# Optimization experiments

Measured on AMD Instinct MI355X. Metric: run time of the kernel, lower is better.

## Reference

```python
import jax, jax.numpy as jnp
import numpy as np

B, POMO, PROB, EMB, H, D = 64, 200, 200, 512, 16, 32
SQRT_EMB = 22.627416997969522  # sqrt(512)
CLIP = 10.0


def _heads(x):
    # (b, n, H*D) -> (b, H, n, D)
    b, n, _ = x.shape
    return x.reshape(b, n, H, D).transpose(0, 2, 1, 3)


def setup_inputs() -> dict:
    key = jax.random.key(0)
    ks = jax.random.split(key, 10)
    s = 1.0 / np.sqrt(EMB)
    return {
        "encoded_nodes": jax.random.normal(ks[0], (B, PROB + 1, EMB), jnp.float32),
        "encoded_q1": jax.random.normal(ks[1], (B, POMO, EMB), jnp.float32),
        "encoded_last_node": jax.random.normal(ks[2], (B, POMO, EMB), jnp.float32),
        "ninf_mask": jnp.zeros((B, POMO, PROB), jnp.float32),
        "Wq_first": jax.random.normal(ks[3], (EMB, H * D), jnp.float32) * s,
        "Wq_last": jax.random.normal(ks[4], (EMB, H * D), jnp.float32) * s,
        "Wk": jax.random.normal(ks[5], (EMB, H * D), jnp.float32) * s,
        "Wv": jax.random.normal(ks[6], (EMB, H * D), jnp.float32) * s,
        "Wc": jax.random.normal(ks[7], (H * D, EMB), jnp.float32) * s,
        "bc": jax.random.normal(ks[8], (EMB,), jnp.float32) * 0.01,
    }


def reference(encoded_nodes, encoded_q1, encoded_last_node, ninf_mask,
              Wq_first, Wq_last, Wk, Wv, Wc, bc):
    # set_kv
    k = _heads(encoded_nodes @ Wk)            # (b, H, prob+1, D)
    v = _heads(encoded_nodes @ Wv)            # (b, H, prob+1, D)
    single_head_key = encoded_nodes[:, :-1]   # (b, prob, emb)
    # set_q1 + forward queries
    q = _heads(encoded_q1 @ Wq_first) + _heads(encoded_last_node @ Wq_last)  # (b, H, pomo, D)
    # masked multi-head attention; mask padded with a zero column for the depot/last node
    mask3 = jnp.concatenate([ninf_mask, jnp.zeros((B, POMO, 1), ninf_mask.dtype)], axis=-1)
    score = jnp.einsum('bhnd,bhmd->bhnm', q, k) / jnp.sqrt(jnp.float32(D))
    weights = jax.nn.softmax(score + mask3[:, None, :, :], axis=-1)
    out = jnp.einsum('bhnm,bhmd->bhnd', weights, v)        # (b, H, pomo, D)
    out_concat = out.transpose(0, 2, 1, 3).reshape(B, POMO, H * D)
    mh_atten_out = out_concat @ Wc + bc                    # (b, pomo, emb)
    # single-head pointer score with tanh clipping
    score2 = jnp.einsum('bne,bpe->bnp', mh_atten_out, single_head_key) / SQRT_EMB
    score_masked = CLIP * jnp.tanh(score2) + ninf_mask
    return jax.nn.softmax(score_masked, axis=2)            # (b, pomo, prob)
```

## Files before the change

kernel.cpp:

```cpp
#include <hip/hip_runtime.h>
#include <cstdint>
#include <cstddef>

typedef _Float16 f16;
typedef f16 f16x4 __attribute__((ext_vector_type(4)));
typedef f16 f16x8 __attribute__((ext_vector_type(8)));
typedef float f32x4 __attribute__((ext_vector_type(4)));

#define NB    64
#define NPOMO 200
#define NNODE 201
#define NEMB  512
#define NH    16
#define ND    32

__device__ __forceinline__ void gload16(const void* g, void* l) {
  __builtin_amdgcn_global_load_lds((const __attribute__((address_space(1))) void*)g,
                                   (__attribute__((address_space(3))) void*)l, 16, 0, 0);
}


__global__ void cast_x(const float* __restrict__ x, f16* __restrict__ o, int n4) {
  int i = blockIdx.x * 256 + threadIdx.x;
  if (i < n4) {
    float4 v = ((const float4*)x)[i];
    f16x4 h = {(f16)v.x, (f16)v.y, (f16)v.z, (f16)v.w};
    ((f16x4*)o)[i] = h;
  }
}

__global__ void build_qcat(const float* __restrict__ q1, const float* __restrict__ ql,
                           f16* __restrict__ o) {
  int i = blockIdx.x * 256 + threadIdx.x;
  if (i >= 12800 * 256) return;
  int row = i >> 8;
  int g = i & 255;
  const float* src = (g < 128) ? (q1 + (size_t)row * 512 + g * 4)
                               : (ql + (size_t)row * 512 + (g - 128) * 4);
  float4 v = *(const float4*)src;
  f16x4 h = {(f16)v.x, (f16)v.y, (f16)v.z, (f16)v.w};
  ((f16x4*)o)[i] = h;
}

__global__ void build_w(const float* __restrict__ Wk, const float* __restrict__ Wv,
                        const float* __restrict__ Wqf, const float* __restrict__ Wql,
                        const float* __restrict__ Wc,
                        f16* __restrict__ wkvT, f16* __restrict__ wqT, f16* __restrict__ wcT) {
  int i = blockIdx.x * 256 + threadIdx.x;
  if (i < 524288) {
    int j = i >> 9, k = i & 511;
    float v = (j < 512) ? Wk[(size_t)k * 512 + j] : Wv[(size_t)k * 512 + (j - 512)];
    wkvT[i] = (f16)v;
  } else if (i < 1048576) {
    int t = i - 524288;
    int j = t >> 10, k = t & 1023;
    float v = (k < 512) ? Wqf[(size_t)k * 512 + j] : Wql[(size_t)(k - 512) * 512 + j];
    wqT[t] = (f16)v;
  } else if (i < 1310720) {
    int t = i - 1048576;
    int j = t >> 9, k = t & 511;
    wcT[t] = (f16)Wc[(size_t)k * 512 + j];
  }
}


__global__ __launch_bounds__(256, 2) void gemm_tn(
    const f16* __restrict__ A, const f16* __restrict__ B, f16* __restrict__ C,
    const float* __restrict__ bias, int M, int N, int K) {
  __shared__ f16 As[128 * 64];
  __shared__ f16 Bs[128 * 64];
  const int tid = threadIdx.x;
  const int wave = tid >> 6, lane = tid & 63;
  const int qd = lane >> 4, c = lane & 15;
  const int wm = wave >> 1, wn = wave & 1;
  const int m0 = blockIdx.x * 128, n0 = blockIdx.y * 128;
  const int srow = lane >> 3, sj = lane & 7;

  f32x4 acc[4][4];
#pragma unroll
  for (int i = 0; i < 4; ++i)
#pragma unroll
    for (int j = 0; j < 4; ++j) acc[i][j] = (f32x4){0.f, 0.f, 0.f, 0.f};

  for (int kc = 0; kc < K; kc += 64) {
#pragma unroll
    for (int i = 0; i < 4; ++i) {
      int row = wave * 32 + i * 8 + srow;
      int gr = m0 + row; if (gr >= M) gr = M - 1;
      int gj = sj ^ (row & 7);
      gload16(A + (size_t)gr * K + kc + gj * 8, As + row * 64 + sj * 8);
    }
#pragma unroll
    for (int i = 0; i < 4; ++i) {
      int row = wave * 32 + i * 8 + srow;
      int gj = sj ^ (row & 7);
      gload16(B + (size_t)(n0 + row) * K + kc + gj * 8, Bs + row * 64 + sj * 8);
    }
    __syncthreads();
#pragma unroll
    for (int kk = 0; kk < 2; ++kk) {
      f16x8 af[4], bf[4];
#pragma unroll
      for (int t = 0; t < 4; ++t) {
        int ra = wm * 64 + t * 16 + c;
        af[t] = *(const f16x8*)(As + ra * 64 + (((kk * 4 + qd) ^ (ra & 7)) * 8));
        int rb = wn * 64 + t * 16 + c;
        bf[t] = *(const f16x8*)(Bs + rb * 64 + (((kk * 4 + qd) ^ (rb & 7)) * 8));
      }
#pragma unroll
      for (int mt = 0; mt < 4; ++mt)
#pragma unroll
        for (int nt = 0; nt < 4; ++nt)
          acc[mt][nt] = __builtin_amdgcn_mfma_f32_16x16x32_f16(af[mt], bf[nt], acc[mt][nt], 0, 0, 0);
    }
    __syncthreads();
  }

#pragma unroll
  for (int mt = 0; mt < 4; ++mt) {
#pragma unroll
    for (int nt = 0; nt < 4; ++nt) {
      int col = n0 + wn * 64 + nt * 16 + c;
      float bv = bias ? bias[col] : 0.0f;
#pragma unroll
      for (int r = 0; r < 4; ++r) {
        int row = m0 + wm * 64 + mt * 16 + qd * 4 + r;
        if (row < M) C[(size_t)row * N + col] = (f16)(acc[mt][nt][r] + bv);
      }
    }
  }
}


#define VSTR 268

__global__ __launch_bounds__(256, 4) void attn_kernel(
    const f16* __restrict__ Qp, const f16* __restrict__ KV,
    const float* __restrict__ mask, f16* __restrict__ Oc) {
  __shared__ f16 Vt[32 * VSTR];
  const int bid = blockIdx.x;
  const int qq = bid & 3;
  const int h = (bid >> 2) & 15;
  const int b = bid >> 6;
  const int tid = threadIdx.x;
  const int wave = tid >> 6, lane = tid & 63;
  const int qd = lane >> 4, c = lane & 15;

  for (int idx = tid; idx < 208 * 8; idx += 256) {
    int m = idx >> 3, ch = idx & 7;
    f16x4 v = (f16x4){0, 0, 0, 0};
    if (m < 201) v = *(const f16x4*)(KV + ((size_t)(b * NNODE + m)) * 1024 + 512 + h * 32 + ch * 4);
    Vt[(ch * 4 + 0) * VSTR + m] = v.x;
    Vt[(ch * 4 + 1) * VSTR + m] = v.y;
    Vt[(ch * 4 + 2) * VSTR + m] = v.z;
    Vt[(ch * 4 + 3) * VSTR + m] = v.w;
  }
  __syncthreads();

  const int start = (qq == 0) ? 0 : (1 + 3 * qq);
  const int ntile = (qq == 0) ? 4 : 3;
  const int rt = start + wave;
  if (wave >= ntile) return;

  const int r0 = rt * 16;
  const int qrow = min(r0 + c, 199);
  const float scale = 0.17677669529663687f;

  f16x8 aq = *(const f16x8*)(Qp + ((size_t)(b * NPOMO + qrow)) * 512 + h * 32 + qd * 8);

  f32x4 s[13];
#pragma unroll
  for (int nt = 0; nt < 13; ++nt) {
    int node = nt * 16 + c; if (node > 200) node = 200;
    f16x8 ak = *(const f16x8*)(KV + ((size_t)(b * NNODE + node)) * 1024 + h * 32 + qd * 8);
    f32x4 z = (f32x4){0.f, 0.f, 0.f, 0.f};
    s[nt] = __builtin_amdgcn_mfma_f32_16x16x32_f16(ak, aq, z, 0, 0, 0);
  }

  float mx = -3e38f;
#pragma unroll
  for (int nt = 0; nt < 13; ++nt) {
    const int col0 = nt * 16 + qd * 4;
    float4 mv = make_float4(0.f, 0.f, 0.f, 0.f);
    if (col0 < 200)
      mv = *(const float4*)(mask + ((size_t)b * NPOMO + qrow) * 200 + col0);
#pragma unroll
    for (int r = 0; r < 4; ++r) {
      int node = col0 + r;
      float v;
      if (node > 200)      v = -3e38f;
      else if (node == 200) v = s[nt][r] * scale;
      else                  v = s[nt][r] * scale + ((const float*)&mv)[r];
      s[nt][r] = v;
      mx = fmaxf(mx, v);
    }
  }
  mx = fmaxf(mx, __shfl_xor(mx, 16));
  mx = fmaxf(mx, __shfl_xor(mx, 32));

  float sm = 0.f;
  f16x4 pf[13];
#pragma unroll
  for (int nt = 0; nt < 13; ++nt) {
    f16x4 p4;
#pragma unroll
    for (int r = 0; r < 4; ++r) {
      float p = __expf(s[nt][r] - mx);
      sm += p;
      p4[r] = (f16)p;
    }
    pf[nt] = p4;
  }
  sm += __shfl_xor(sm, 16);
  sm += __shfl_xor(sm, 32);
  const float inv = 1.0f / sm;

  f32x4 o0 = (f32x4){0.f, 0.f, 0.f, 0.f};
  f32x4 o1 = (f32x4){0.f, 0.f, 0.f, 0.f};
#pragma unroll
  for (int nt = 0; nt < 13; ++nt) {
    const int nb = nt * 16 + qd * 4;
    f16x4 av0 = *(const f16x4*)(Vt + c * VSTR + nb);
    f16x4 av1 = *(const f16x4*)(Vt + (c + 16) * VSTR + nb);
    o0 = __builtin_amdgcn_mfma_f32_16x16x16f16(av0, pf[nt], o0, 0, 0, 0);
    o1 = __builtin_amdgcn_mfma_f32_16x16x16f16(av1, pf[nt], o1, 0, 0, 0);
  }

  const int row = r0 + c;
  if (row < 200) {
    f16* dst = Oc + ((size_t)(b * NPOMO + row)) * 512 + h * 32 + qd * 4;
    f16x4 w0 = {(f16)(o0[0] * inv), (f16)(o0[1] * inv), (f16)(o0[2] * inv), (f16)(o0[3] * inv)};
    f16x4 w1 = {(f16)(o1[0] * inv), (f16)(o1[1] * inv), (f16)(o1[2] * inv), (f16)(o1[3] * inv)};
    *(f16x4*)dst = w0;
    *(f16x4*)(dst + 16) = w1;
  }
}


__global__ __launch_bounds__(256, 2) void final_kernel(
    const f16* __restrict__ mh, const f16* __restrict__ Xnh,
    const float* __restrict__ mask, float* __restrict__ out) {
  __shared__ f16 As[64 * 72];
  __shared__ f16 Bs[208 * 72];
  const int b = blockIdx.x >> 2, rb = blockIdx.x & 3;
  const int r0 = rb * 64;
  const int tid = threadIdx.x;
  const int wave = tid >> 6, lane = tid & 63;
  const int qd = lane >> 4, c = lane & 15;

  f32x4 acc[13];
#pragma unroll
  for (int i = 0; i < 13; ++i) acc[i] = (f32x4){0.f, 0.f, 0.f, 0.f};

  for (int kc = 0; kc < 512; kc += 64) {
    for (int idx = tid; idx < 64 * 16; idx += 256) {
      int row = idx >> 4, ch = idx & 15;
      int gr = r0 + row; if (gr > 199) gr = 199;
      *(f16x4*)(As + row * 72 + ch * 4) =
          *(const f16x4*)(mh + ((size_t)b * NPOMO + gr) * 512 + kc + ch * 4);
    }
    for (int idx = tid; idx < 208 * 16; idx += 256) {
      int n = idx >> 4, ch = idx & 15;
      f16x4 v = (f16x4){0, 0, 0, 0};
      if (n < 200) v = *(const f16x4*)(Xnh + ((size_t)b * NNODE + n) * 512 + kc + ch * 4);
      *(f16x4*)(Bs + n * 72 + ch * 4) = v;
    }
    __syncthreads();
#pragma unroll
    for (int kk = 0; kk < 2; ++kk) {
      f16x8 a = *(const f16x8*)(As + (wave * 16 + c) * 72 + kk * 32 + qd * 8);
#pragma unroll
      for (int nt = 0; nt < 13; ++nt) {
        f16x8 bb = *(const f16x8*)(Bs + (nt * 16 + c) * 72 + kk * 32 + qd * 8);
        acc[nt] = __builtin_amdgcn_mfma_f32_16x16x32_f16(a, bb, acc[nt], 0, 0, 0);
      }
    }
    __syncthreads();
  }

  const float invS = 1.0f / 22.627416997969522f;
  const int rowb = r0 + wave * 16 + qd * 4;
  float mx[4] = {-3e38f, -3e38f, -3e38f, -3e38f};
#pragma unroll
  for (int nt = 0; nt < 13; ++nt) {
    int col = nt * 16 + c;
#pragma unroll
    for (int r = 0; r < 4; ++r) {
      float v;
      if (col < 200) {
        v = 10.0f * tanhf(acc[nt][r] * invS);
        int rr = rowb + r;
        if (rr < 200) v += mask[((size_t)b * NPOMO + rr) * 200 + col];
      } else {
        v = -3e38f;
      }
      acc[nt][r] = v;
      mx[r] = fmaxf(mx[r], v);
    }
  }
#pragma unroll
  for (int off = 8; off >= 1; off >>= 1)
#pragma unroll
    for (int r = 0; r < 4; ++r) mx[r] = fmaxf(mx[r], __shfl_xor(mx[r], off, 16));
  float sm[4] = {0.f, 0.f, 0.f, 0.f};
#pragma unroll
  for (int nt = 0; nt < 13; ++nt)
#pragma unroll
    for (int r = 0; r < 4; ++r) {
      float p = __expf(acc[nt][r] - mx[r]);
      acc[nt][r] = p;
      sm[r] += p;
    }
#pragma unroll
  for (int off = 8; off >= 1; off >>= 1)
#pragma unroll
    for (int r = 0; r < 4; ++r) sm[r] += __shfl_xor(sm[r], off, 16);
  float inv[4];
#pragma unroll
  for (int r = 0; r < 4; ++r) inv[r] = 1.0f / sm[r];
#pragma unroll
  for (int nt = 0; nt < 13; ++nt) {
    int col = nt * 16 + c;
#pragma unroll
    for (int r = 0; r < 4; ++r) {
      int rr = rowb + r;
      if (col < 200 && rr < 200)
        out[((size_t)b * NPOMO + rr) * 200 + col] = acc[nt][r] * inv[r];
    }
  }
}


extern "C" void kernel_launch(void* const* d_in, const int* in_sizes, int n_in,
                              void* d_out, int out_size, void* d_ws, size_t ws_size,
                              hipStream_t stream) {
  (void)in_sizes; (void)n_in; (void)out_size; (void)ws_size;
  const float* enc   = (const float*)d_in[0];
  const float* q1    = (const float*)d_in[1];
  const float* qlast = (const float*)d_in[2];
  const float* mask  = (const float*)d_in[3];
  const float* Wqf   = (const float*)d_in[4];
  const float* Wql   = (const float*)d_in[5];
  const float* Wk    = (const float*)d_in[6];
  const float* Wv    = (const float*)d_in[7];
  const float* Wc    = (const float*)d_in[8];
  const float* bc    = (const float*)d_in[9];
  float* out = (float*)d_out;

  char* ws = (char*)d_ws;
  f16* Xnh  = (f16*)(ws + 0);
  f16* Qcat = (f16*)(ws + 13172736);
  f16* WkvT = (f16*)(ws + 39387136);
  f16* WqT  = (f16*)(ws + 40435712);
  f16* WcT  = (f16*)(ws + 41484288);
  f16* KVp  = (f16*)(ws + 42008576);
  f16* Qp   = (f16*)(ws + 68354048);
  f16* Oc   = (f16*)(ws + 81461248);
  f16* mhb  = (f16*)(ws + 94568448);

  hipLaunchKernelGGL(cast_x, dim3(6432), dim3(256), 0, stream, enc, Xnh, 1646592);
  hipLaunchKernelGGL(build_qcat, dim3(12800), dim3(256), 0, stream, q1, qlast, Qcat);
  hipLaunchKernelGGL(build_w, dim3(5120), dim3(256), 0, stream, Wk, Wv, Wqf, Wql, Wc, WkvT, WqT, WcT);
  hipLaunchKernelGGL(gemm_tn, dim3(101, 8), dim3(256), 0, stream,
                     Xnh, WkvT, KVp, (const float*)nullptr, 12864, 1024, 512);
  hipLaunchKernelGGL(gemm_tn, dim3(100, 4), dim3(256), 0, stream,
                     Qcat, WqT, Qp, (const float*)nullptr, 12800, 512, 1024);
  hipLaunchKernelGGL(attn_kernel, dim3(4096), dim3(256), 0, stream, Qp, KVp, mask, Oc);
  hipLaunchKernelGGL(gemm_tn, dim3(100, 4), dim3(256), 0, stream,
                     Oc, WcT, mhb, bc, 12800, 512, 512);
  hipLaunchKernelGGL(final_kernel, dim3(256), dim3(256), 0, stream, mhb, Xnh, mask, out);
}
```

Before: 351.6 us.

## Restructure final pointer-score kernel into 16-row tiles with direct global MFMA loads

The final kernel now launches 13 blocks per batch, each handling 16 query rows, instead of 4 blocks of 64 rows. The node columns are split across the four waves. Operands are read straight from global memory into MFMA registers rather than staged through LDS, and the row softmax reduction runs across waves through small shared arrays. tanh is computed with an exp-based formula, and mask loads and output stores become float4. This raises the block count from 256 to 832 to fill more compute units, at the cost of re-reading the node keys once per tile and using uncoalesced global loads.

Measured after the change: 316.2 us. 1.11x faster.

```diff
diff --git a/kernel.cpp b/kernel.cpp
--- a/kernel.cpp
+++ b/kernel.cpp
@@ -237,95 +237,109 @@
 }
 
 
-__global__ __launch_bounds__(256, 2) void final_kernel(
+__global__ __launch_bounds__(256, 4) void final_kernel(
     const f16* __restrict__ mh, const f16* __restrict__ Xnh,
     const float* __restrict__ mask, float* __restrict__ out) {
-  __shared__ f16 As[64 * 72];
-  __shared__ f16 Bs[208 * 72];
-  const int b = blockIdx.x >> 2, rb = blockIdx.x & 3;
-  const int r0 = rb * 64;
+  __shared__ float xmax[4][16];
+  __shared__ float xsum[4][16];
+  const int b = blockIdx.x / 13;
+  const int tile = blockIdx.x % 13;
+  const int r0 = tile * 16;
   const int tid = threadIdx.x;
   const int wave = tid >> 6, lane = tid & 63;
   const int qd = lane >> 4, c = lane & 15;
 
-  f32x4 acc[13];
-#pragma unroll
-  for (int i = 0; i < 13; ++i) acc[i] = (f32x4){0.f, 0.f, 0.f, 0.f};
-
-  for (int kc = 0; kc < 512; kc += 64) {
-    for (int idx = tid; idx < 64 * 16; idx += 256) {
-      int row = idx >> 4, ch = idx & 15;
-      int gr = r0 + row; if (gr > 199) gr = 199;
-      *(f16x4*)(As + row * 72 + ch * 4) =
-          *(const f16x4*)(mh + ((size_t)b * NPOMO + gr) * 512 + kc + ch * 4);
-    }
-    for (int idx = tid; idx < 208 * 16; idx += 256) {
-      int n = idx >> 4, ch = idx & 15;
-      f16x4 v = (f16x4){0, 0, 0, 0};
-      if (n < 200) v = *(const f16x4*)(Xnh + ((size_t)b * NNODE + n) * 512 + kc + ch * 4);
-      *(f16x4*)(Bs + n * 72 + ch * 4) = v;
-    }
-    __syncthreads();
-#pragma unroll
-    for (int kk = 0; kk < 2; ++kk) {
-      f16x8 a = *(const f16x8*)(As + (wave * 16 + c) * 72 + kk * 32 + qd * 8);
-#pragma unroll
-      for (int nt = 0; nt < 13; ++nt) {
-        f16x8 bb = *(const f16x8*)(Bs + (nt * 16 + c) * 72 + kk * 32 + qd * 8);
-        acc[nt] = __builtin_amdgcn_mfma_f32_16x16x32_f16(a, bb, acc[nt], 0, 0, 0);
-      }
-    }
-    __syncthreads();
+  const int nt0 = (wave == 0) ? 0 : (3 * wave + 1);
+  const int cnt = (wave == 0) ? 4 : 3;
+
+  const int qrow = min(r0 + c, 199);
+  const size_t rbase = ((size_t)(b * NPOMO + qrow)) * 512;
+
+  size_t abase[4];
+#pragma unroll
+  for (int i = 0; i < 4; ++i) {
+    int nt = nt0 + i;
+    int nd = nt * 16 + c; if (nd > 200) nd = 200;
+    abase[i] = ((size_t)(b * NNODE + nd)) * 512;
+  }
+
+  f32x4 acc[4];
+#pragma unroll
+  for (int i = 0; i < 4; ++i) acc[i] = (f32x4){0.f, 0.f, 0.f, 0.f};
+
+#pragma unroll 4
+  for (int kc = 0; kc < 512; kc += 32) {
+    f16x8 bq = *(const f16x8*)(mh + rbase + kc + qd * 8);
+#pragma unroll
+    for (int i = 0; i < 4; ++i) {
+      if (i < cnt) {
+        f16x8 a = *(const f16x8*)(Xnh + abase[i] + kc + qd * 8);
+        acc[i] = __builtin_amdgcn_mfma_f32_16x16x32_f16(a, bq, acc[i], 0, 0, 0);
+      }
+    }
   }
 
   const float invS = 1.0f / 22.627416997969522f;
-  const int rowb = r0 + wave * 16 + qd * 4;
-  float mx[4] = {-3e38f, -3e38f, -3e38f, -3e38f};
-#pragma unroll
-  for (int nt = 0; nt < 13; ++nt) {
-    int col = nt * 16 + c;
+  float mx = -3e38f;
+#pragma unroll
+  for (int i = 0; i < 4; ++i) {
+    if (i >= cnt) break;
+    const int nt = nt0 + i;
+    const int col0 = nt * 16 + qd * 4;
+    float4 mv = make_float4(0.f, 0.f, 0.f, 0.f);
+    if (col0 < 200)
+      mv = *(const float4*)(mask + ((size_t)b * NPOMO + qrow) * 200 + col0);
 #pragma unroll
     for (int r = 0; r < 4; ++r) {
+      int node = col0 + r;
       float v;
-      if (col < 200) {
-        v = 10.0f * tanhf(acc[nt][r] * invS);
-        int rr = rowb + r;
-        if (rr < 200) v += mask[((size_t)b * NPOMO + rr) * 200 + col];
+      if (node < 200) {
+        float t = __expf(2.0f * acc[i][r] * invS);
+        float th = 1.0f - 2.0f / (t + 1.0f);
+        v = 10.0f * th + ((const float*)&mv)[r];
       } else {
         v = -3e38f;
       }
-      acc[nt][r] = v;
-      mx[r] = fmaxf(mx[r], v);
-    }
-  }
-#pragma unroll
-  for (int off = 8; off >= 1; off >>= 1)
-#pragma unroll
-    for (int r = 0; r < 4; ++r) mx[r] = fmaxf(mx[r], __shfl_xor(mx[r], off, 16));
-  float sm[4] = {0.f, 0.f, 0.f, 0.f};
-#pragma unroll
-  for (int nt = 0; nt < 13; ++nt)
+      acc[i][r] = v;
+      mx = fmaxf(mx, v);
+    }
+  }
+  mx = fmaxf(mx, __shfl_xor(mx, 16));
+  mx = fmaxf(mx, __shfl_xor(mx, 32));
+  if (lane < 16) xmax[wave][lane] = mx;
+  __syncthreads();
+  mx = fmaxf(fmaxf(xmax[0][c], xmax[1][c]), fmaxf(xmax[2][c], xmax[3][c]));
+
+  float sm = 0.f;
+#pragma unroll
+  for (int i = 0; i < 4; ++i) {
+    if (i >= cnt) break;
 #pragma unroll
     for (int r = 0; r < 4; ++r) {
-      float p = __expf(acc[nt][r] - mx[r]);
-      acc[nt][r] = p;
-      sm[r] += p;
-    }
-#pragma unroll
-  for (int off = 8; off >= 1; off >>= 1)
-#pragma unroll
-    for (int r = 0; r < 4; ++r) sm[r] += __shfl_xor(sm[r], off, 16);
-  float inv[4];
-#pragma unroll
-  for (int r = 0; r < 4; ++r) inv[r] = 1.0f / sm[r];
-#pragma unroll
-  for (int nt = 0; nt < 13; ++nt) {
-    int col = nt * 16 + c;
-#pragma unroll
-    for (int r = 0; r < 4; ++r) {
-      int rr = rowb + r;
-      if (col < 200 && rr < 200)
-        out[((size_t)b * NPOMO + rr) * 200 + col] = acc[nt][r] * inv[r];
+      float p = __expf(acc[i][r] - mx);
+      acc[i][r] = p;
+      sm += p;
+    }
+  }
+  sm += __shfl_xor(sm, 16);
+  sm += __shfl_xor(sm, 32);
+  if (lane < 16) xsum[wave][lane] = sm;
+  __syncthreads();
+  const float tot = xsum[0][c] + xsum[1][c] + xsum[2][c] + xsum[3][c];
+  const float inv = 1.0f / tot;
+
+  const int row = r0 + c;
+  if (row < 200) {
+#pragma unroll
+    for (int i = 0; i < 4; ++i) {
+      if (i >= cnt) break;
+      const int col0 = (nt0 + i) * 16 + qd * 4;
+      if (col0 < 200) {
+        float4 o;
+        o.x = acc[i][0] * inv; o.y = acc[i][1] * inv;
+        o.z = acc[i][2] * inv; o.w = acc[i][3] * inv;
+        *(float4*)(out + ((size_t)b * NPOMO + row) * 200 + col0) = o;
+      }
     }
   }
 }
@@ -368,5 +382,5 @@
   hipLaunchKernelGGL(attn_kernel, dim3(4096), dim3(256), 0, stream, Qp, KVp, mask, Oc);
   hipLaunchKernelGGL(gemm_tn, dim3(100, 4), dim3(256), 0, stream,
                      Oc, WcT, mhb, bc, 12800, 512, 512);
-  hipLaunchKernelGGL(final_kernel, dim3(256), dim3(256), 0, stream, mhb, Xnh, mask, out);
-}
+  hipLaunchKernelGGL(final_kernel, dim3(832), dim3(256), 0, stream, mhb, Xnh, mask, out);
+}
```
